# Kernel tuning notes

Hardware: AMD Instinct MI355X
Metric: run time of the kernel (lower is better)

## Reference

```python
import jax, jax.numpy as jnp
import numpy as np

B, T, S, A, H = 64, 1000, 96, 32, 256
INP = S + A  # 128


def setup_inputs() -> dict:
    key = jax.random.key(0)
    ks = jax.random.split(key, 20)
    def xavier(k, shape):
        fan_in, fan_out = shape[0], shape[1]
        lim = jnp.sqrt(6.0 / (fan_in + fan_out))
        return jax.random.uniform(k, shape, jnp.float32, -lim, lim)
    return {
        "state": jax.random.normal(ks[0], (B, T, S), jnp.float32),
        "action": jax.random.normal(ks[1], (B, T, A), jnp.float32),
        "hn": jnp.zeros((1, B, H), jnp.float32),
        # branch 1 params
        "fc11_w": xavier(ks[2], (INP, H)),
        "fc11_b": jnp.zeros((H,), jnp.float32),
        "W_hh1": xavier(ks[3], (H, H)),
        "W_ih1": xavier(ks[4], (H, H)),
        "b_hh1": jax.random.uniform(ks[5], (H,), jnp.float32),
        "b_ih1": jax.random.uniform(ks[6], (H,), jnp.float32),
        "fc12_w": xavier(ks[7], (H, 1)),
        "fc12_b": jnp.zeros((1,), jnp.float32),
        # branch 2 params
        "fc21_w": xavier(ks[8], (INP, H)),
        "fc21_b": jnp.zeros((H,), jnp.float32),
        "W_hh2": xavier(ks[9], (H, H)),
        "W_ih2": xavier(ks[10], (H, H)),
        "b_hh2": jax.random.uniform(ks[11], (H,), jnp.float32),
        "b_ih2": jax.random.uniform(ks[12], (H,), jnp.float32),
        "fc22_w": xavier(ks[13], (H, 1)),
        "fc22_b": jnp.zeros((1,), jnp.float32),
    }


def _rnn_branch(x, h0, W_hh, W_ih, b_hh, b_ih):
    # x: [B, T, H] (post input projection + relu); h0: [B, H]
    bias = b_hh + b_ih
    def step(h, x_t):
        h_next = jax.nn.sigmoid(h @ W_hh + x_t @ W_ih + bias)
        return h_next, h_next
    xs = jnp.swapaxes(x, 0, 1)  # [T, B, H]
    _, hs = jax.lax.scan(step, h0, xs)
    return jnp.swapaxes(hs, 0, 1)  # [B, T, H]


def reference(state, action, hn, fc11_w, fc11_b, W_hh1, W_ih1, b_hh1, b_ih1,
              fc12_w, fc12_b, fc21_w, fc21_b, W_hh2, W_ih2, b_hh2, b_ih2,
              fc22_w, fc22_b):
    x = jnp.concatenate((state, action), axis=-1)  # [B, T, INP]
    h0 = hn[0]  # squeeze(0) -> [B, H]

    x1 = jax.nn.relu(x @ fc11_w + fc11_b)
    rnn1 = _rnn_branch(x1, h0, W_hh1, W_ih1, b_hh1, b_ih1)
    q1 = rnn1 @ fc12_w + fc12_b  # [B, T, 1]

    x2 = jax.nn.relu(x @ fc21_w + fc21_b)
    rnn2 = _rnn_branch(x2, h0, W_hh2, W_ih2, b_hh2, b_ih2)
    q2 = rnn2 @ fc22_w + fc22_b  # [B, T, 1]

    return (q1, q2)
```

## Files before the change

### kernel.cpp

```cpp
#include <hip/hip_runtime.h>
#include <math.h>


typedef _Float16 half2_t __attribute__((ext_vector_type(2)));
typedef __attribute__((ext_vector_type(8))) short bf16x8;
typedef __attribute__((ext_vector_type(4))) float f32x4;

__device__ __forceinline__ float fdot2(half2_t a, half2_t b, float c) {
#if __has_builtin(__builtin_amdgcn_fdot2)
    return __builtin_amdgcn_fdot2(a, b, c, false);
#else
    return c + (float)a[0] * (float)b[0] + (float)a[1] * (float)b[1];
#endif
}

__device__ __forceinline__ short f2bf(float f) {
    unsigned u = __builtin_bit_cast(unsigned, f);
    return (short)((u + 0x7FFFu + ((u >> 16) & 1u)) >> 16);
}

__device__ __forceinline__ void barrier_lds() {
    __asm__ __volatile__("s_waitcnt lgkmcnt(0)" ::: "memory");
    __builtin_amdgcn_s_barrier();
}

__global__ __launch_bounds__(256, 1)
void prep_kernel(const float* __restrict__ fc11_w, const float* __restrict__ W_ih1,
                 const float* __restrict__ fc21_w, const float* __restrict__ W_ih2,
                 short* __restrict__ tab)
{
    const int e    = blockIdx.x * 256 + threadIdx.x;
    const int lane = e & 63;
    const int q = lane >> 4, m = lane & 15;
    const float* W;
    int k0, n;
    if (e < 8192) {
        int t_ = e >> 6;
        int ks = t_ & 3, nt = (t_ >> 2) & 15, br = t_ >> 6;
        W = br ? fc21_w : fc11_w;
        k0 = ks * 32 + q * 8; n = nt * 16 + m;
    } else {
        int t_ = (e - 8192) >> 6;
        int ks = t_ & 7, nt = (t_ >> 3) & 15, br = t_ >> 7;
        W = br ? W_ih2 : W_ih1;
        k0 = ks * 32 + q * 8; n = nt * 16 + m;
    }
    bf16x8 v;
#pragma unroll
    for (int j = 0; j < 8; ++j) v[j] = f2bf(W[(size_t)(k0 + j) * 256 + n]);
    ((bf16x8*)tab)[e] = v;
}

__global__ __launch_bounds__(256, 2)
void ff_kernel(const float* __restrict__ state,
               const float* __restrict__ action,
               const float* __restrict__ fc11_b, const float* __restrict__ fc21_b,
               const float* __restrict__ b_hh1, const float* __restrict__ b_ih1,
               const float* __restrict__ b_hh2, const float* __restrict__ b_ih2,
               const short* __restrict__ tab,
               _Float16* __restrict__ pre_out)
{
    __shared__ short X1[128 * 264];

    const int tile = blockIdx.x % 500;
    const int br   = blockIdx.x / 500;
    const int tid  = threadIdx.x;
    const int w    = tid >> 6;
    const int lane = tid & 63;
    const int q = lane >> 4, m = lane & 15;
    const int row0 = tile * 128;

    const float* ba = br ? fc21_b : fc11_b;
    const float* bh = br ? b_hh2 : b_hh1;
    const float* bi = br ? b_ih2 : b_ih1;
    const bf16x8* tG1 = (const bf16x8*)tab + (size_t)br * 4096;
    const bf16x8* tG2 = (const bf16x8*)tab + 8192 + (size_t)br * 8192;

    float ba_v[16], bb_v[16];
#pragma unroll
    for (int nt = 0; nt < 16; ++nt) {
        int c = nt * 16 + m;
        ba_v[nt] = ba[c];
        bb_v[nt] = bh[c] + bi[c];
    }

    bf16x8 af[2][4];
#pragma unroll
    for (int mt = 0; mt < 2; ++mt) {
        const int rw = row0 + 64 * mt + 16 * w + m;
#pragma unroll
        for (int ks = 0; ks < 4; ++ks) {
            int k0 = ks * 32 + q * 8;
            const float* src = (k0 < 96) ? (state  + (size_t)rw * 96 + k0)
                                         : (action + (size_t)rw * 32 + (k0 - 96));
            float4 x0 = *(const float4*)src;
            float4 x1 = *(const float4*)(src + 4);
            bf16x8 a;
            a[0] = f2bf(x0.x); a[1] = f2bf(x0.y); a[2] = f2bf(x0.z); a[3] = f2bf(x0.w);
            a[4] = f2bf(x1.x); a[5] = f2bf(x1.y); a[6] = f2bf(x1.z); a[7] = f2bf(x1.w);
            af[mt][ks] = a;
        }
    }

#pragma unroll 4
    for (int nt = 0; nt < 16; ++nt) {
        bf16x8 bf[4];
#pragma unroll
        for (int ks = 0; ks < 4; ++ks) bf[ks] = tG1[(nt * 4 + ks) * 64 + lane];
#pragma unroll
        for (int mt = 0; mt < 2; ++mt) {
            f32x4 acc = {0.f, 0.f, 0.f, 0.f};
#pragma unroll
            for (int ks = 0; ks < 4; ++ks)
                acc = __builtin_amdgcn_mfma_f32_16x16x32_bf16(af[mt][ks], bf[ks], acc, 0, 0, 0);
#pragma unroll
            for (int r = 0; r < 4; ++r) {
                float v = acc[r] + ba_v[nt];
                v = v > 0.f ? v : 0.f;
                X1[(64 * mt + 16 * w + q * 4 + r) * 264 + nt * 16 + m] = f2bf(v);
            }
        }
    }

    bf16x8 a2[2][8];
#pragma unroll
    for (int mt = 0; mt < 2; ++mt)
#pragma unroll
        for (int ks = 0; ks < 8; ++ks)
            a2[mt][ks] = *(const bf16x8*)&X1[(64 * mt + 16 * w + m) * 264 + ks * 32 + q * 8];

    _Float16* pre = pre_out + (size_t)br * 64000u * 256u;
#pragma unroll 2
    for (int nt = 0; nt < 16; ++nt) {
        bf16x8 bg[8];
#pragma unroll
        for (int ks = 0; ks < 8; ++ks) bg[ks] = tG2[(nt * 8 + ks) * 64 + lane];
#pragma unroll
        for (int mt = 0; mt < 2; ++mt) {
            f32x4 acc = {0.f, 0.f, 0.f, 0.f};
#pragma unroll
            for (int ks = 0; ks < 8; ++ks)
                acc = __builtin_amdgcn_mfma_f32_16x16x32_bf16(a2[mt][ks], bg[ks], acc, 0, 0, 0);
#pragma unroll
            for (int r = 0; r < 4; ++r) {
                float v = acc[r] + bb_v[nt];
                pre[(size_t)(row0 + 64 * mt + 16 * w + q * 4 + r) * 256 + nt * 16 + m] = (_Float16)v;
            }
        }
    }
}

__global__ __launch_bounds__(256)
__attribute__((amdgpu_waves_per_eu(1, 1)))
void rnn_kernel(const _Float16* __restrict__ pre_all,
                const float* __restrict__ hn,
                const float* __restrict__ W_hh1,
                const float* __restrict__ W_hh2,
                _Float16* __restrict__ h_out)
{
    __shared__ _Float16 hbuf[2][256];

    const int wg = blockIdx.x;
    const int br = wg >> 6;
    const int b  = wg & 63;
    const float* Whh = br ? W_hh2 : W_hh1;
    const _Float16* pre = pre_all + ((size_t)br * 64000u + (size_t)b * 1000u) * 256u;
    _Float16* hg = h_out + ((size_t)br * 64000u + (size_t)b * 1000u) * 256u;

    const int t = threadIdx.x;

    unsigned whb[128];
#pragma unroll
    for (int i = 0; i < 128; ++i) {
        float lo = Whh[(size_t)(2 * i)     * 256 + t];
        float hi = Whh[(size_t)(2 * i + 1) * 256 + t];
        whb[i] = __builtin_bit_cast(unsigned, half2_t{(_Float16)lo, (_Float16)hi});
    }
#pragma unroll
    for (int i = 0; i < 128; ++i)
        __asm__ __volatile__("" : "+v"(whb[i]));

    hbuf[0][t] = (_Float16)hn[b * 256 + t];
    barrier_lds();

    float pre_c = (float)pre[t];
    float pre_n = (float)pre[256 + t];

    for (int tt = 0; tt < 1000; ++tt) {
        const int t2 = (tt + 2 < 1000) ? (tt + 2) : 999;
        const float pre_n2 = (float)pre[(size_t)t2 * 256 + t];

        const int pp = tt & 1;
        const float4* hb = (const float4*)&hbuf[pp][0];

        float sA0 = 0.f, sA1 = 0.f, sA2 = 0.f, sA3 = 0.f;
        float sB0 = 0.f, sB1 = 0.f, sB2 = 0.f, sB3 = 0.f;
#pragma unroll
        for (int j = 0; j < 32; ++j) {
            float4 v = hb[j];
            const half2_t* hh = (const half2_t*)&v;
#define WH(idx) __builtin_bit_cast(half2_t, whb[idx])
            if (j & 1) {
                sB0 = fdot2(hh[0], WH(4 * j + 0), sB0);
                sB1 = fdot2(hh[1], WH(4 * j + 1), sB1);
                sB2 = fdot2(hh[2], WH(4 * j + 2), sB2);
                sB3 = fdot2(hh[3], WH(4 * j + 3), sB3);
            } else {
                sA0 = fdot2(hh[0], WH(4 * j + 0), sA0);
                sA1 = fdot2(hh[1], WH(4 * j + 1), sA1);
                sA2 = fdot2(hh[2], WH(4 * j + 2), sA2);
                sA3 = fdot2(hh[3], WH(4 * j + 3), sA3);
            }
#undef WH
        }

        const float z = (((sA0 + sA1) + (sA2 + sA3)) +
                         ((sB0 + sB1) + (sB2 + sB3))) + pre_c;
        const float h = 1.0f / (1.0f + __expf(-z));
        const _Float16 h16 = (_Float16)h;
        hbuf[pp ^ 1][t] = h16;
        hg[(size_t)tt * 256 + t] = h16;
        barrier_lds();

        pre_c = pre_n;
        pre_n = pre_n2;
    }
}

__global__ __launch_bounds__(256, 2)
void q_kernel(const _Float16* __restrict__ h_all,
              const float* __restrict__ fc12_w, const float* __restrict__ fc12_b,
              const float* __restrict__ fc22_w, const float* __restrict__ fc22_b,
              float* __restrict__ out)
{
    const int n  = blockIdx.x * 256 + threadIdx.x;
    const int br = (n >= 64000);
    const float* qwp = br ? fc22_w : fc12_w;
    const float  qb  = br ? fc22_b[0] : fc12_b[0];

    half2_t qw[128];
#pragma unroll
    for (int i = 0; i < 128; ++i)
        qw[i] = half2_t{(_Float16)qwp[2 * i], (_Float16)qwp[2 * i + 1]};

    const float4* hr = (const float4*)(h_all + (size_t)n * 256u);
    float s0 = qb, s1 = 0.f, s2 = 0.f, s3 = 0.f;
#pragma unroll
    for (int k = 0; k < 32; ++k) {
        float4 v = hr[k];
        const half2_t* hh = (const half2_t*)&v;
        s0 = fdot2(hh[0], qw[4 * k + 0], s0);
        s1 = fdot2(hh[1], qw[4 * k + 1], s1);
        s2 = fdot2(hh[2], qw[4 * k + 2], s2);
        s3 = fdot2(hh[3], qw[4 * k + 3], s3);
    }
    out[n] = (s0 + s1) + (s2 + s3);
}

extern "C" void kernel_launch(void* const* d_in, const int* in_sizes, int n_in,
                              void* d_out, int out_size, void* d_ws, size_t ws_size,
                              hipStream_t stream)
{
    const float* state  = (const float*)d_in[0];
    const float* action = (const float*)d_in[1];
    const float* hn     = (const float*)d_in[2];
    const float* fc11_w = (const float*)d_in[3];
    const float* fc11_b = (const float*)d_in[4];
    const float* W_hh1  = (const float*)d_in[5];
    const float* W_ih1  = (const float*)d_in[6];
    const float* b_hh1  = (const float*)d_in[7];
    const float* b_ih1  = (const float*)d_in[8];
    const float* fc12_w = (const float*)d_in[9];
    const float* fc12_b = (const float*)d_in[10];
    const float* fc21_w = (const float*)d_in[11];
    const float* fc21_b = (const float*)d_in[12];
    const float* W_hh2  = (const float*)d_in[13];
    const float* W_ih2  = (const float*)d_in[14];
    const float* b_hh2  = (const float*)d_in[15];
    const float* b_ih2  = (const float*)d_in[16];
    const float* fc22_w = (const float*)d_in[17];
    const float* fc22_b = (const float*)d_in[18];

    _Float16* pre = (_Float16*)d_ws;
    _Float16* hbg = (_Float16*)d_ws + 32768000u;
    short* tab = (short*)((char*)d_ws + 130678784u);

    prep_kernel<<<96, 256, 0, stream>>>(fc11_w, W_ih1, fc21_w, W_ih2, tab);
    ff_kernel<<<1000, 256, 0, stream>>>(state, action,
                                        fc11_b, fc21_b, b_hh1, b_ih1,
                                        b_hh2, b_ih2, tab, pre);
    rnn_kernel<<<128, 256, 0, stream>>>(pre, hn, W_hh1, W_hh2, hbg);
    q_kernel<<<500, 256, 0, stream>>>(hbg, fc12_w, fc12_b, fc22_w, fc22_b,
                                      (float*)d_out);
}
```

Measured before the change: 819.2 us.

## Batch 16 sequences per RNN workgroup using f16 MFMA for the recurrence

The recurrent step changes from one workgroup per sequence doing fdot2 matvecs to one workgroup per 16 sequences doing 16x16x32 f16 MFMA. W_hh is pre-packed into MFMA fragment layout held in registers. The ff and q kernels are changed to write and read a matching tiled layout for pre-activations and hidden states, and the q kernel now reduces with shuffles and LDS. Only 8 workgroups run the serial 1000-step loop instead of 128, which trades parallelism for far fewer instructions per step, so per-step MFMA latency and barrier cost now set the pace.

```diff
diff --git a/kernel.cpp b/kernel.cpp
--- a/kernel.cpp
+++ b/kernel.cpp
@@ -3,6 +3,8 @@
 
 
 typedef _Float16 half2_t __attribute__((ext_vector_type(2)));
+typedef _Float16 f16x8   __attribute__((ext_vector_type(8)));
+typedef _Float16 f16x16  __attribute__((ext_vector_type(16)));
 typedef __attribute__((ext_vector_type(8))) short bf16x8;
 typedef __attribute__((ext_vector_type(4))) float f32x4;
 
@@ -27,28 +29,41 @@
 __global__ __launch_bounds__(256, 1)
 void prep_kernel(const float* __restrict__ fc11_w, const float* __restrict__ W_ih1,
                  const float* __restrict__ fc21_w, const float* __restrict__ W_ih2,
-                 short* __restrict__ tab)
+                 const float* __restrict__ W_hh1, const float* __restrict__ W_hh2,
+                 short* __restrict__ tab, _Float16* __restrict__ tab3)
 {
     const int e    = blockIdx.x * 256 + threadIdx.x;
     const int lane = e & 63;
     const int q = lane >> 4, m = lane & 15;
-    const float* W;
-    int k0, n;
-    if (e < 8192) {
-        int t_ = e >> 6;
-        int ks = t_ & 3, nt = (t_ >> 2) & 15, br = t_ >> 6;
-        W = br ? fc21_w : fc11_w;
-        k0 = ks * 32 + q * 8; n = nt * 16 + m;
+    if (e < 24576) {
+        const float* W;
+        int k0, n;
+        if (e < 8192) {
+            int t_ = e >> 6;
+            int ks = t_ & 3, nt = (t_ >> 2) & 15, br = t_ >> 6;
+            W = br ? fc21_w : fc11_w;
+            k0 = ks * 32 + q * 8; n = nt * 16 + m;
+        } else {
+            int t_ = (e - 8192) >> 6;
+            int ks = t_ & 7, nt = (t_ >> 3) & 15, br = t_ >> 7;
+            W = br ? W_ih2 : W_ih1;
+            k0 = ks * 32 + q * 8; n = nt * 16 + m;
+        }
+        bf16x8 v;
+#pragma unroll
+        for (int j = 0; j < 8; ++j) v[j] = f2bf(W[(size_t)(k0 + j) * 256 + n]);
+        ((bf16x8*)tab)[e] = v;
     } else {
-        int t_ = (e - 8192) >> 6;
-        int ks = t_ & 7, nt = (t_ >> 3) & 15, br = t_ >> 7;
-        W = br ? W_ih2 : W_ih1;
-        k0 = ks * 32 + q * 8; n = nt * 16 + m;
-    }
-    bf16x8 v;
-#pragma unroll
-    for (int j = 0; j < 8; ++j) v[j] = f2bf(W[(size_t)(k0 + j) * 256 + n]);
-    ((bf16x8*)tab)[e] = v;
+        int e3 = e - 24576;
+        int t_ = e3 >> 6;
+        int ks = t_ & 7, nt = (t_ >> 3) & 15, brr = t_ >> 7;
+        const float* W = brr ? W_hh2 : W_hh1;
+        int k0 = ks * 32 + q * 8, n = nt * 16 + m;
+        f16x8 v;
+#pragma unroll
+        for (int j = 0; j < 8; ++j) v[j] = (_Float16)W[(size_t)(k0 + j) * 256 + n];
+        ((f16x8*)tab3)[e3] = v;
+    }
 }
 
 __global__ __launch_bounds__(256, 2)
@@ -129,24 +144,49 @@
         for (int ks = 0; ks < 8; ++ks)
             a2[mt][ks] = *(const bf16x8*)&X1[(64 * mt + 16 * w + m) * 264 + ks * 32 + q * 8];
 
-    _Float16* pre = pre_out + (size_t)br * 64000u * 256u;
-#pragma unroll 2
-    for (int nt = 0; nt < 16; ++nt) {
-        bf16x8 bg[8];
-#pragma unroll
-        for (int ks = 0; ks < 8; ++ks) bg[ks] = tG2[(nt * 8 + ks) * 64 + lane];
-#pragma unroll
-        for (int mt = 0; mt < 2; ++mt) {
-            f32x4 acc = {0.f, 0.f, 0.f, 0.f};
-#pragma unroll
-            for (int ks = 0; ks < 8; ++ks)
-                acc = __builtin_amdgcn_mfma_f32_16x16x32_bf16(a2[mt][ks], bg[ks], acc, 0, 0, 0);
+    size_t hbase[2][4];
+#pragma unroll
+    for (int mt = 0; mt < 2; ++mt)
+#pragma unroll
+        for (int r = 0; r < 4; ++r) {
+            unsigned row = (unsigned)(row0 + 64 * mt + 16 * w + q * 4 + r);
+            unsigned b = row / 1000u;
+            unsigned t = row - b * 1000u;
+            unsigned G = b >> 4, g2 = (b >> 2) & 3, rr = b & 3;
+            hbase[mt][r] = (size_t)(((unsigned)br * 4u + G) * 1000u + t) * 4096u
+                         + (size_t)(g2 * 16 + m) * 16u + rr * 4u;
+        }
+
+#pragma unroll
+    for (int wv = 0; wv < 4; ++wv) {
+        f32x4 accq[2][4];
+#pragma unroll
+        for (int tl = 0; tl < 4; ++tl) {
+            const int nt = wv * 4 + tl;
+            bf16x8 bg[8];
+#pragma unroll
+            for (int ks = 0; ks < 8; ++ks) bg[ks] = tG2[(nt * 8 + ks) * 64 + lane];
+#pragma unroll
+            for (int mt = 0; mt < 2; ++mt) {
+                f32x4 acc = {0.f, 0.f, 0.f, 0.f};
+#pragma unroll
+                for (int ks = 0; ks < 8; ++ks)
+                    acc = __builtin_amdgcn_mfma_f32_16x16x32_bf16(a2[mt][ks], bg[ks], acc, 0, 0, 0);
+                accq[mt][tl] = acc;
+            }
+        }
+#pragma unroll
+        for (int mt = 0; mt < 2; ++mt)
 #pragma unroll
             for (int r = 0; r < 4; ++r) {
-                float v = acc[r] + bb_v[nt];
-                pre[(size_t)(row0 + 64 * mt + 16 * w + q * 4 + r) * 256 + nt * 16 + m] = (_Float16)v;
+                half2_t p0 = {(_Float16)(accq[mt][0][r] + bb_v[wv * 4 + 0]),
+                              (_Float16)(accq[mt][1][r] + bb_v[wv * 4 + 1])};
+                half2_t p1 = {(_Float16)(accq[mt][2][r] + bb_v[wv * 4 + 2]),
+                              (_Float16)(accq[mt][3][r] + bb_v[wv * 4 + 3])};
+                uint2 pk = {__builtin_bit_cast(unsigned, p0),
+                            __builtin_bit_cast(unsigned, p1)};
+                *(uint2*)(pre_out + hbase[mt][r] + (size_t)wv * 1024u) = pk;
             }
-        }
     }
 }
 
@@ -154,107 +194,136 @@
 __attribute__((amdgpu_waves_per_eu(1, 1)))
 void rnn_kernel(const _Float16* __restrict__ pre_all,
                 const float* __restrict__ hn,
-                const float* __restrict__ W_hh1,
-                const float* __restrict__ W_hh2,
+                const _Float16* __restrict__ tab3,
                 _Float16* __restrict__ h_out)
 {
-    __shared__ _Float16 hbuf[2][256];
+    __shared__ _Float16 hl[2][16][264];
 
     const int wg = blockIdx.x;
-    const int br = wg >> 6;
-    const int b  = wg & 63;
-    const float* Whh = br ? W_hh2 : W_hh1;
-    const _Float16* pre = pre_all + ((size_t)br * 64000u + (size_t)b * 1000u) * 256u;
-    _Float16* hg = h_out + ((size_t)br * 64000u + (size_t)b * 1000u) * 256u;
-
-    const int t = threadIdx.x;
-
-    unsigned whb[128];
-#pragma unroll
-    for (int i = 0; i < 128; ++i) {
-        float lo = Whh[(size_t)(2 * i)     * 256 + t];
-        float hi = Whh[(size_t)(2 * i + 1) * 256 + t];
-        whb[i] = __builtin_bit_cast(unsigned, half2_t{(_Float16)lo, (_Float16)hi});
-    }
-#pragma unroll
-    for (int i = 0; i < 128; ++i)
-        __asm__ __volatile__("" : "+v"(whb[i]));
-
-    hbuf[0][t] = (_Float16)hn[b * 256 + t];
+    const int br = wg >> 2;
+    const int G  = wg & 3;
+    const int tid = threadIdx.x;
+    const int wv = tid >> 6, l = tid & 63;
+    const int g2 = l >> 4, m = l & 15;
+
+    f16x8 wfr[4][8];
+#pragma unroll
+    for (int tl = 0; tl < 4; ++tl)
+#pragma unroll
+        for (int ks = 0; ks < 8; ++ks) {
+            const int nt = wv * 4 + tl;
+            wfr[tl][ks] = ((const f16x8*)tab3)[(((size_t)br * 16 + nt) * 8 + ks) * 64 + l];
+        }
+#pragma unroll
+    for (int tl = 0; tl < 4; ++tl)
+#pragma unroll
+        for (int ks = 0; ks < 8; ++ks)
+            __asm__ __volatile__("" : "+v"(wfr[tl][ks]));
+
+    {
+        const int seq = tid >> 4, nc = (tid & 15) * 16;
+        const float* src = hn + (size_t)(G * 16 + seq) * 256 + nc;
+#pragma unroll
+        for (int j = 0; j < 16; ++j) hl[0][seq][nc + j] = (_Float16)src[j];
+    }
     barrier_lds();
 
-    float pre_c = (float)pre[t];
-    float pre_n = (float)pre[256 + t];
+    const size_t slab0 = (size_t)(br * 4 + G) * 1000u;
+    f16x16 pc = *(const f16x16*)(pre_all + (slab0 + 0) * 4096u + (size_t)tid * 16u);
+    f16x16 pn = *(const f16x16*)(pre_all + (slab0 + 1) * 4096u + (size_t)tid * 16u);
 
     for (int tt = 0; tt < 1000; ++tt) {
         const int t2 = (tt + 2 < 1000) ? (tt + 2) : 999;
-        const float pre_n2 = (float)pre[(size_t)t2 * 256 + t];
+        f16x16 p2 = *(const f16x16*)(pre_all + (slab0 + t2) * 4096u + (size_t)tid * 16u);
 
         const int pp = tt & 1;
-        const float4* hb = (const float4*)&hbuf[pp][0];
-
-        float sA0 = 0.f, sA1 = 0.f, sA2 = 0.f, sA3 = 0.f;
-        float sB0 = 0.f, sB1 = 0.f, sB2 = 0.f, sB3 = 0.f;
-#pragma unroll
-        for (int j = 0; j < 32; ++j) {
-            float4 v = hb[j];
-            const half2_t* hh = (const half2_t*)&v;
-#define WH(idx) __builtin_bit_cast(half2_t, whb[idx])
-            if (j & 1) {
-                sB0 = fdot2(hh[0], WH(4 * j + 0), sB0);
-                sB1 = fdot2(hh[1], WH(4 * j + 1), sB1);
-                sB2 = fdot2(hh[2], WH(4 * j + 2), sB2);
-                sB3 = fdot2(hh[3], WH(4 * j + 3), sB3);
-            } else {
-                sA0 = fdot2(hh[0], WH(4 * j + 0), sA0);
-                sA1 = fdot2(hh[1], WH(4 * j + 1), sA1);
-                sA2 = fdot2(hh[2], WH(4 * j + 2), sA2);
-                sA3 = fdot2(hh[3], WH(4 * j + 3), sA3);
+
+        f16x8 a[8];
+#pragma unroll
+        for (int ks = 0; ks < 8; ++ks)
+            a[ks] = *(const f16x8*)&hl[pp][m][ks * 32 + g2 * 8];
+
+        f32x4 acc[4];
+#pragma unroll
+        for (int tl = 0; tl < 4; ++tl)
+#pragma unroll
+            for (int r = 0; r < 4; ++r)
+                acc[tl][r] = (float)pc[r * 4 + tl];
+#pragma unroll
+        for (int ks = 0; ks < 8; ++ks)
+#pragma unroll
+            for (int tl = 0; tl < 4; ++tl)
+                acc[tl] = __builtin_amdgcn_mfma_f32_16x16x32_f16(a[ks], wfr[tl][ks], acc[tl], 0, 0, 0);
+
+        unsigned hp[8];
+#pragma unroll
+        for (int r = 0; r < 4; ++r)
+#pragma unroll
+            for (int tp = 0; tp < 2; ++tp) {
+                const int tl0 = 2 * tp;
+                float h0 = 1.0f / (1.0f + __expf(-acc[tl0 + 0][r]));
+                float h1 = 1.0f / (1.0f + __expf(-acc[tl0 + 1][r]));
+                half2_t h2 = {(_Float16)h0, (_Float16)h1};
+                hp[r * 2 + tp] = __builtin_bit_cast(unsigned, h2);
+                hl[pp ^ 1][g2 * 4 + r][wv * 64 + (tl0 + 0) * 16 + m] = h2[0];
+                hl[pp ^ 1][g2 * 4 + r][wv * 64 + (tl0 + 1) * 16 + m] = h2[1];
             }
-#undef WH
-        }
-
-        const float z = (((sA0 + sA1) + (sA2 + sA3)) +
-                         ((sB0 + sB1) + (sB2 + sB3))) + pre_c;
-        const float h = 1.0f / (1.0f + __expf(-z));
-        const _Float16 h16 = (_Float16)h;
-        hbuf[pp ^ 1][t] = h16;
-        hg[(size_t)tt * 256 + t] = h16;
+        _Float16* hgp = h_out + (slab0 + tt) * 4096u + (size_t)tid * 16u;
+        *(uint4*)hgp       = uint4{hp[0], hp[1], hp[2], hp[3]};
+        *(uint4*)(hgp + 8) = uint4{hp[4], hp[5], hp[6], hp[7]};
+
         barrier_lds();
-
-        pre_c = pre_n;
-        pre_n = pre_n2;
-    }
-}
-
-__global__ __launch_bounds__(256, 2)
+        pc = pn; pn = p2;
+    }
+}
+
+__global__ __launch_bounds__(256, 4)
 void q_kernel(const _Float16* __restrict__ h_all,
               const float* __restrict__ fc12_w, const float* __restrict__ fc12_b,
               const float* __restrict__ fc22_w, const float* __restrict__ fc22_b,
               float* __restrict__ out)
 {
-    const int n  = blockIdx.x * 256 + threadIdx.x;
-    const int br = (n >= 64000);
+    __shared__ float part[4][4][4];
+    const int sb  = blockIdx.x;
+    const int br  = sb / 4000;
+    const int rem = sb - br * 4000;
+    const int G   = rem / 1000;
+    const int t   = rem - G * 1000;
+    const int tid = threadIdx.x;
+    const int wv = tid >> 6, l = tid & 63, g2 = l >> 4, m = l & 15;
     const float* qwp = br ? fc22_w : fc12_w;
-    const float  qb  = br ? fc22_b[0] : fc12_b[0];
-
-    half2_t qw[128];
-#pragma unroll
-    for (int i = 0; i < 128; ++i)
-        qw[i] = half2_t{(_Float16)qwp[2 * i], (_Float16)qwp[2 * i + 1]};
-
-    const float4* hr = (const float4*)(h_all + (size_t)n * 256u);
-    float s0 = qb, s1 = 0.f, s2 = 0.f, s3 = 0.f;
-#pragma unroll
-    for (int k = 0; k < 32; ++k) {
-        float4 v = hr[k];
-        const half2_t* hh = (const half2_t*)&v;
-        s0 = fdot2(hh[0], qw[4 * k + 0], s0);
-        s1 = fdot2(hh[1], qw[4 * k + 1], s1);
-        s2 = fdot2(hh[2], qw[4 * k + 2], s2);
-        s3 = fdot2(hh[3], qw[4 * k + 3], s3);
-    }
-    out[n] = (s0 + s1) + (s2 + s3);
+
+    f16x16 hv = *(const f16x16*)(h_all + (size_t)sb * 4096u + (size_t)tid * 16u);
+    half2_t q01 = {(_Float16)qwp[wv * 64 + 0 * 16 + m], (_Float16)qwp[wv * 64 + 1 * 16 + m]};
+    half2_t q23 = {(_Float16)qwp[wv * 64 + 2 * 16 + m], (_Float16)qwp[wv * 64 + 3 * 16 + m]};
+
+    float s0, s1, s2, s3;
+    {
+        half2_t a0 = {hv[0],  hv[1]},  b0 = {hv[2],  hv[3]};
+        half2_t a1 = {hv[4],  hv[5]},  b1 = {hv[6],  hv[7]};
+        half2_t a2 = {hv[8],  hv[9]},  b2 = {hv[10], hv[11]};
+        half2_t a3 = {hv[12], hv[13]}, b3 = {hv[14], hv[15]};
+        s0 = fdot2(b0, q23, fdot2(a0, q01, 0.f));
+        s1 = fdot2(b1, q23, fdot2(a1, q01, 0.f));
+        s2 = fdot2(b2, q23, fdot2(a2, q01, 0.f));
+        s3 = fdot2(b3, q23, fdot2(a3, q01, 0.f));
+    }
+#pragma unroll
+    for (int off = 1; off < 16; off <<= 1) {
+        s0 += __shfl_xor(s0, off, 64);
+        s1 += __shfl_xor(s1, off, 64);
+        s2 += __shfl_xor(s2, off, 64);
+        s3 += __shfl_xor(s3, off, 64);
+    }
+    if (m == 0) *(float4*)&part[wv][g2][0] = float4{s0, s1, s2, s3};
+    __syncthreads();
+    if (tid < 16) {
+        const int gg = tid >> 2, rr = tid & 3;
+        float q = (part[0][gg][rr] + part[1][gg][rr]) +
+                  (part[2][gg][rr] + part[3][gg][rr]) +
+                  (br ? fc22_b[0] : fc12_b[0]);
+        out[(size_t)br * 64000u + (size_t)(G * 16 + gg * 4 + rr) * 1000u + t] = q;
+    }
 }
 
 extern "C" void kernel_launch(void* const* d_in, const int* in_sizes, int n_in,
@@ -281,15 +350,17 @@
     const float* fc22_w = (const float*)d_in[17];
     const float* fc22_b = (const float*)d_in[18];
 
-    _Float16* pre = (_Float16*)d_ws;
-    _Float16* hbg = (_Float16*)d_ws + 32768000u;
-    short* tab = (short*)((char*)d_ws + 130678784u);
-
-    prep_kernel<<<96, 256, 0, stream>>>(fc11_w, W_ih1, fc21_w, W_ih2, tab);
+    _Float16* pre  = (_Float16*)d_ws;
+    _Float16* hbg  = (_Float16*)d_ws + 32768000u;
+    _Float16* tab3 = (_Float16*)((char*)d_ws + 130416640u);
+    short*    tab  = (short*)((char*)d_ws + 130678784u);
+
+    prep_kernel<<<160, 256, 0, stream>>>(fc11_w, W_ih1, fc21_w, W_ih2,
+                                         W_hh1, W_hh2, tab, tab3);
     ff_kernel<<<1000, 256, 0, stream>>>(state, action,
                                         fc11_b, fc21_b, b_hh1, b_ih1,
                                         b_hh2, b_ih2, tab, pre);
-    rnn_kernel<<<128, 256, 0, stream>>>(pre, hn, W_hh1, W_hh2, hbg);
-    q_kernel<<<500, 256, 0, stream>>>(hbg, fc12_w, fc12_b, fc22_w, fc22_b,
-                                      (float*)d_out);
-}
+    rnn_kernel<<<8, 256, 0, stream>>>(pre, hn, tab3, hbg);
+    q_kernel<<<8000, 256, 0, stream>>>(hbg, fc12_w, fc12_b, fc22_w, fc22_b,
+                                       (float*)d_out);
+}
```

New measurement: 1.238 ms. 51.1% more time.

## Pack two RNN sequences per 512-thread block and unroll recurrence by two

Applied to the files above, without the earlier changes.

The RNN kernel now runs two independent batch sequences in one 512-thread workgroup (64 blocks instead of 128), each with its own double-buffered LDS hidden state. The timestep loop is unrolled by two with a macro, and prefetch of the pre-activation is reduced to two rotating 16-bit registers. The idea is to let two waves per SIMD interleave their serial dot-product and barrier latency. In exchange, the barriers now sync both sequences together, and the register budget per wave is squeezed by waves_per_eu(2,2) while 128 weight registers must still fit.

```diff
diff --git a/kernel.cpp b/kernel.cpp
--- a/kernel.cpp
+++ b/kernel.cpp
@@ -150,24 +150,25 @@
     }
 }
 
-__global__ __launch_bounds__(256)
-__attribute__((amdgpu_waves_per_eu(1, 1)))
+__global__ __launch_bounds__(512)
+__attribute__((amdgpu_waves_per_eu(2, 2)))
 void rnn_kernel(const _Float16* __restrict__ pre_all,
                 const float* __restrict__ hn,
                 const float* __restrict__ W_hh1,
                 const float* __restrict__ W_hh2,
                 _Float16* __restrict__ h_out)
 {
-    __shared__ _Float16 hbuf[2][256];
-
-    const int wg = blockIdx.x;
-    const int br = wg >> 6;
-    const int b  = wg & 63;
+    __shared__ _Float16 hbuf[2][2][256];
+
+    const int tid = threadIdx.x;
+    const int sl  = tid >> 8;
+    const int t   = tid & 255;
+    const int s   = blockIdx.x * 2 + sl;
+    const int br  = s >> 6;
+    const int b   = s & 63;
     const float* Whh = br ? W_hh2 : W_hh1;
     const _Float16* pre = pre_all + ((size_t)br * 64000u + (size_t)b * 1000u) * 256u;
     _Float16* hg = h_out + ((size_t)br * 64000u + (size_t)b * 1000u) * 256u;
-
-    const int t = threadIdx.x;
 
     unsigned whb[128];
 #pragma unroll
@@ -176,55 +177,58 @@
         float hi = Whh[(size_t)(2 * i + 1) * 256 + t];
         whb[i] = __builtin_bit_cast(unsigned, half2_t{(_Float16)lo, (_Float16)hi});
     }
-#pragma unroll
-    for (int i = 0; i < 128; ++i)
-        __asm__ __volatile__("" : "+v"(whb[i]));
-
-    hbuf[0][t] = (_Float16)hn[b * 256 + t];
+
+    hbuf[sl][0][t] = (_Float16)hn[b * 256 + t];
     barrier_lds();
 
-    float pre_c = (float)pre[t];
-    float pre_n = (float)pre[256 + t];
-
-    for (int tt = 0; tt < 1000; ++tt) {
+    unsigned short pA = *(const unsigned short*)(pre + t);
+    unsigned short pB = *(const unsigned short*)(pre + 256 + t);
+
+#define WH(idx) __builtin_bit_cast(half2_t, whb[idx])
+#define RSTEP(P, PR, TT, T2)                                                  \
+    {                                                                         \
+        const float4* hb = (const float4*)&hbuf[sl][P][0];                    \
+        float sA0 = 0.f, sA1 = 0.f, sA2 = 0.f, sA3 = 0.f;                     \
+        float sB0 = 0.f, sB1 = 0.f, sB2 = 0.f, sB3 = 0.f;                     \
+        _Pragma("unroll")                                                     \
+        for (int j = 0; j < 32; ++j) {                                        \
+            float4 v = hb[j];                        \
+            const half2_t* hh = (const half2_t*)&v;                           \
+            if (j & 1) {                                                      \
+                sB0 = fdot2(hh[0], WH(4 * j + 0), sB0);                       \
+                sB1 = fdot2(hh[1], WH(4 * j + 1), sB1);                       \
+                sB2 = fdot2(hh[2], WH(4 * j + 2), sB2);                       \
+                sB3 = fdot2(hh[3], WH(4 * j + 3), sB3);                       \
+            } else {                                                          \
+                sA0 = fdot2(hh[0], WH(4 * j + 0), sA0);                       \
+                sA1 = fdot2(hh[1], WH(4 * j + 1), sA1);                       \
+                sA2 = fdot2(hh[2], WH(4 * j + 2), sA2);                       \
+                sA3 = fdot2(hh[3], WH(4 * j + 3), sA3);                       \
+            }                                                                 \
+        }                                                                     \
+        const float z = (((sA0 + sA1) + (sA2 + sA3)) +                        \
+                         ((sB0 + sB1) + (sB2 + sB3))) +                       \
+                        (float)__builtin_bit_cast(_Float16, PR);              \
+        PR = *(const unsigned short*)(pre + (size_t)(T2) * 256 + t);          \
+        const float h = 1.0f / (1.0f + __expf(-z));                           \
+        const _Float16 h16 = (_Float16)h;                                     \
+        hbuf[sl][(P) ^ 1][t] = h16;                                           \
+        hg[(size_t)(TT) * 256 + t] = h16;       \
+        barrier_lds();                           \
+    }
+
+    for (int tt = 0; tt < 1000; tt += 2) {
+#pragma unroll
+        for (int i = 0; i < 128; ++i)
+            __asm__ __volatile__("" : "+v"(whb[i]));
+
         const int t2 = (tt + 2 < 1000) ? (tt + 2) : 999;
-        const float pre_n2 = (float)pre[(size_t)t2 * 256 + t];
-
-        const int pp = tt & 1;
-        const float4* hb = (const float4*)&hbuf[pp][0];
-
-        float sA0 = 0.f, sA1 = 0.f, sA2 = 0.f, sA3 = 0.f;
-        float sB0 = 0.f, sB1 = 0.f, sB2 = 0.f, sB3 = 0.f;
-#pragma unroll
-        for (int j = 0; j < 32; ++j) {
-            float4 v = hb[j];
-            const half2_t* hh = (const half2_t*)&v;
-#define WH(idx) __builtin_bit_cast(half2_t, whb[idx])
-            if (j & 1) {
-                sB0 = fdot2(hh[0], WH(4 * j + 0), sB0);
-                sB1 = fdot2(hh[1], WH(4 * j + 1), sB1);
-                sB2 = fdot2(hh[2], WH(4 * j + 2), sB2);
-                sB3 = fdot2(hh[3], WH(4 * j + 3), sB3);
-            } else {
-                sA0 = fdot2(hh[0], WH(4 * j + 0), sA0);
-                sA1 = fdot2(hh[1], WH(4 * j + 1), sA1);
-                sA2 = fdot2(hh[2], WH(4 * j + 2), sA2);
-                sA3 = fdot2(hh[3], WH(4 * j + 3), sA3);
-            }
+        RSTEP(0, pA, tt, t2)
+        const int t3 = (tt + 3 < 1000) ? (tt + 3) : 999;
+        RSTEP(1, pB, tt + 1, t3)
+    }
+#undef RSTEP
 #undef WH
-        }
-
-        const float z = (((sA0 + sA1) + (sA2 + sA3)) +
-                         ((sB0 + sB1) + (sB2 + sB3))) + pre_c;
-        const float h = 1.0f / (1.0f + __expf(-z));
-        const _Float16 h16 = (_Float16)h;
-        hbuf[pp ^ 1][t] = h16;
-        hg[(size_t)tt * 256 + t] = h16;
-        barrier_lds();
-
-        pre_c = pre_n;
-        pre_n = pre_n2;
-    }
 }
 
 __global__ __launch_bounds__(256, 2)
@@ -289,7 +293,7 @@
     ff_kernel<<<1000, 256, 0, stream>>>(state, action,
                                         fc11_b, fc21_b, b_hh1, b_ih1,
                                         b_hh2, b_ih2, tab, pre);
-    rnn_kernel<<<128, 256, 0, stream>>>(pre, hn, W_hh1, W_hh2, hbg);
+    rnn_kernel<<<64, 512, 0, stream>>>(pre, hn, W_hh1, W_hh2, hbg);
     q_kernel<<<500, 256, 0, stream>>>(hbg, fc12_w, fc12_b, fc22_w, fc22_b,
                                       (float*)d_out);
 }
```

Result: slower. 1.085 ms (+32.5%).
